# Optimization experiments

Measured on AMD Instinct MI355X. Metric: run time of the kernel, lower is better.

## Reference

```python
import jax, jax.numpy as jnp
import numpy as np

FEAT = 128
N_RBF = 20
CUTOFF = 5.0
NUM_CONV = 3
N_ATOMS = 8000
N_EDGES = 160000
N_MOLS = 100
EPS = 1e-15


def silu(x):
    return x * jax.nn.sigmoid(x)


def setup_inputs() -> dict:
    key = jax.random.key(0)
    ks = jax.random.split(key, 16)
    F = FEAT

    def w(k, shape, fan_in):
        return jax.random.normal(k, shape, dtype=jnp.float32) / np.sqrt(fan_in).astype(np.float32)

    nbr0 = jax.random.randint(ks[12], (N_EDGES,), 0, N_ATOMS)
    # avoid self-edges (would give zero distance)
    nbr1 = (nbr0 + 1 + jax.random.randint(ks[13], (N_EDGES,), 0, N_ATOMS - 1)) % N_ATOMS
    return {
        "xyz": jax.random.uniform(ks[0], (N_ATOMS, 3), dtype=jnp.float32) * 10.0,
        "emb_table": jax.random.normal(ks[1], (100, F), dtype=jnp.float32),
        "msg_w1": w(ks[2], (NUM_CONV, F, F), F),
        "msg_b1": jnp.zeros((NUM_CONV, F), jnp.float32),
        "msg_w2": w(ks[3], (NUM_CONV, F, 3 * F), F),
        "msg_b2": jnp.zeros((NUM_CONV, 3 * F), jnp.float32),
        "rbf_w": w(ks[4], (NUM_CONV, N_RBF, 3 * F), N_RBF),
        "rbf_b": jnp.zeros((NUM_CONV, 3 * F), jnp.float32),
        "upd_u": w(ks[5], (NUM_CONV, F, F), F),
        "upd_v": w(ks[6], (NUM_CONV, F, F), F),
        "upd_w1": w(ks[7], (NUM_CONV, 2 * F, F), 2 * F),
        "upd_b1": jnp.zeros((NUM_CONV, F), jnp.float32),
        "upd_w2": w(ks[8], (NUM_CONV, F, 3 * F), F),
        "upd_b2": jnp.zeros((NUM_CONV, 3 * F), jnp.float32),
        "ro_w1": w(ks[9], (F, F // 2), F),
        "ro_b1": jnp.zeros((F // 2,), jnp.float32),
        "ro_w2": w(ks[10], (F // 2, 1), F // 2),
        "ro_b2": jnp.zeros((1,), jnp.float32),
        "z": jax.random.randint(ks[11], (N_ATOMS,), 0, 100),
        "nbrs": jnp.stack([nbr0, nbr1], axis=1),
        "mol_idx": jnp.sort(jax.random.randint(ks[14], (N_ATOMS,), 0, N_MOLS)),
    }


def painn_forward(xyz, emb_table, msg_w1, msg_b1, msg_w2, msg_b2, rbf_w, rbf_b,
                  upd_u, upd_v, upd_w1, upd_b1, upd_w2, upd_b2,
                  ro_w1, ro_b1, ro_w2, ro_b2, z, nbrs, mol_idx):
    F = FEAT
    N = xyz.shape[0]
    # r_ij points from nbrs[:,0] (center i) to nbrs[:,1] (neighbor j)
    r_ij = xyz[nbrs[:, 1]] - xyz[nbrs[:, 0]]            # (E, 3)
    d = jnp.sqrt(jnp.sum(r_ij * r_ij, axis=-1))         # (E,)
    unit = r_ij / d[:, None]                            # (E, 3)
    # PaiNN sinc radial basis: sin(n*pi*d/cutoff)/d, n = 1..n_rbf
    n = jnp.arange(1, N_RBF + 1, dtype=jnp.float32)
    rbf = jnp.sin(n[None, :] * jnp.pi * d[:, None] / CUTOFF) / d[:, None]  # (E, n_rbf)
    # cosine cutoff envelope
    env = jnp.where(d <= CUTOFF, 0.5 * (jnp.cos(jnp.pi * d / CUTOFF) + 1.0), 0.0)

    s = emb_table[z]                                    # (N, F)
    v = jnp.zeros((N, F, 3), dtype=s.dtype)             # (N, F, 3)

    for i in range(NUM_CONV):
        # ---- message block ----
        phi = silu(s @ msg_w1[i] + msg_b1[i]) @ msg_w2[i] + msg_b2[i]   # (N, 3F)
        w_s = (rbf @ rbf_w[i] + rbf_b[i]) * env[:, None]                # (E, 3F)
        inv = (phi[nbrs[:, 1]] * w_s).reshape(-1, 3, F)                 # (E, 3, F)
        split0 = inv[:, 0, :][..., None]                                # (E, F, 1)
        split1 = inv[:, 1, :]                                           # (E, F)
        split2 = inv[:, 2, :][..., None]                                # (E, F, 1)
        dv_ij = split2 * unit[:, None, :] + split0 * v[nbrs[:, 1]]      # (E, F, 3)
        ds = jax.ops.segment_sum(split1, nbrs[:, 0], num_segments=N)
        dv = jax.ops.segment_sum(dv_ij, nbrs[:, 0], num_segments=N)
        s = s + ds
        v = v + dv
        # ---- update block ----
        u_v = jnp.einsum('nfd,fg->ngd', v, upd_u[i])                    # (N, F, 3)
        v_v = jnp.einsum('nfd,fg->ngd', v, upd_v[i])                    # (N, F, 3)
        v_v_norm = jnp.sqrt(jnp.sum(v_v * v_v, axis=-1) + EPS)          # (N, F)
        stack = jnp.concatenate([s, v_v_norm], axis=-1)                 # (N, 2F)
        a = (silu(stack @ upd_w1[i] + upd_b1[i]) @ upd_w2[i] + upd_b2[i]).reshape(-1, 3, F)
        a_vv = a[:, 0, :][..., None]
        a_sv = a[:, 1, :]
        a_ss = a[:, 2, :]
        dv_u = u_v * a_vv
        ds_u = jnp.sum(u_v * v_v, axis=-1) * a_sv + a_ss
        s = s + ds_u
        v = v + dv_u

    # readout MLP + per-molecule sum pool (SumPool)
    atom_e = silu(s @ ro_w1 + ro_b1) @ ro_w2 + ro_b2                    # (N, 1)
    energy = jax.ops.segment_sum(atom_e, mol_idx, num_segments=N_MOLS)  # (N_MOLS, 1)
    return energy


def reference(xyz, emb_table, msg_w1, msg_b1, msg_w2, msg_b2, rbf_w, rbf_b,
              upd_u, upd_v, upd_w1, upd_b1, upd_w2, upd_b2,
              ro_w1, ro_b1, ro_w2, ro_b2, z, nbrs, mol_idx):
    return painn_forward(xyz, emb_table, msg_w1, msg_b1, msg_w2, msg_b2, rbf_w, rbf_b,
                         upd_u, upd_v, upd_w1, upd_b1, upd_w2, upd_b2,
                         ro_w1, ro_b1, ro_w2, ro_b2, z, nbrs, mol_idx)
```

## Files before the change

kernel.cpp:

```cpp
#include <hip/hip_runtime.h>

static constexpr int F = 128;
static constexpr int N_RBF = 20;
static constexpr int N_ATOMS = 8000;
static constexpr int NP = 8064;
static constexpr int N_EDGES = 160000;
static constexpr int N_MOLS = 100;
static constexpr float CUTOFF = 5.0f;
static constexpr size_t NFC = (size_t)NP * F;
static constexpr int REC = 28;
#define PIF 3.14159265358979323846f

typedef __attribute__((ext_vector_type(8))) short bf16x8;
typedef __attribute__((ext_vector_type(4))) float f32x4;
typedef unsigned short ushort_t;
typedef unsigned int uint_t;

__device__ __forceinline__ float silu_f(float x) { return x / (1.f + __expf(-x)); }

__device__ __forceinline__ ushort_t f2bf(float x) {
    union { float f; uint_t u; } v; v.f = x;
    uint_t r = v.u + 0x7fffu + ((v.u >> 16) & 1u);
    return (ushort_t)(r >> 16);
}
__device__ __forceinline__ float bf2f(ushort_t h) {
    union { uint_t u; float f; } v; v.u = ((uint_t)h) << 16; return v.f;
}

__global__ __launch_bounds__(256) void count_kernel(
    const float* __restrict__ xyz, const int* __restrict__ nbrs,
    float* __restrict__ envb, int* __restrict__ cnt)
{
    int e = blockIdx.x * 256 + threadIdx.x;
    if (e >= N_EDGES) return;
    int i0 = nbrs[2*e+0], i1 = nbrs[2*e+1];
    float dx = xyz[3*i1+0] - xyz[3*i0+0];
    float dy = xyz[3*i1+1] - xyz[3*i0+1];
    float dz = xyz[3*i1+2] - xyz[3*i0+2];
    float d  = sqrtf(dx*dx + dy*dy + dz*dz);
    float ev = (d <= CUTOFF) ? 0.5f*(cosf(PIF*d/CUTOFF) + 1.f) : 0.f;
    envb[e] = ev;
    if (ev > 0.f) atomicAdd(&cnt[i0], 1);
}

__global__ __launch_bounds__(1024) void scan_kernel(
    const int* __restrict__ cnt, int* __restrict__ offsets, float* __restrict__ out)
{
    __shared__ int sums[1024];
    int tid = threadIdx.x;
    if (tid < N_MOLS) out[tid] = 0.f;
    int base = tid * 8;
    int local[8]; int s = 0;
    #pragma unroll
    for (int i = 0; i < 8; ++i) {
        int idx = base + i;
        local[i] = (idx < N_ATOMS) ? cnt[idx] : 0;
        s += local[i];
    }
    sums[tid] = s;
    __syncthreads();
    for (int d = 1; d < 1024; d <<= 1) {
        int v = (tid >= d) ? sums[tid - d] : 0;
        __syncthreads();
        sums[tid] += v;
        __syncthreads();
    }
    int ex = (tid == 0) ? 0 : sums[tid - 1];
    #pragma unroll
    for (int i = 0; i < 8; ++i) {
        int idx = base + i;
        if (idx < N_ATOMS) { offsets[idx] = ex; ex += local[i]; }
    }
}

__global__ __launch_bounds__(256) void build_kernel(
    const float* __restrict__ xyz, const int* __restrict__ nbrs,
    const float* __restrict__ envb, const int* __restrict__ offsets,
    int* __restrict__ cursor, float* __restrict__ rec)
{
    int e = blockIdx.x * 256 + threadIdx.x;
    if (e >= N_EDGES) return;
    float ev = envb[e];
    if (ev <= 0.f) return;
    int i0 = nbrs[2*e+0], i1 = nbrs[2*e+1];
    float dx = xyz[3*i1+0] - xyz[3*i0+0];
    float dy = xyz[3*i1+1] - xyz[3*i0+1];
    float dz = xyz[3*i1+2] - xyz[3*i0+2];
    float d  = sqrtf(dx*dx + dy*dy + dz*dz);
    float inv = 1.f / d;
    int pos = offsets[i0] + atomicAdd(&cursor[i0], 1);
    float* r = rec + (size_t)pos * REC;
    r[0] = __int_as_float(i1);
    r[1] = ev;
    r[2] = dx*inv; r[3] = dy*inv; r[4] = dz*inv;
    float base = PIF*d/CUTOFF;
    float sc = inv * ev;
    #pragma unroll
    for (int k = 0; k < N_RBF; ++k)
        r[5 + k] = sinf((float)(k+1)*base) * sc;
}

static constexpr int WPREP_W = 557056;
static constexpr int WPREP_TOTAL = 557184;
static constexpr int NATF = N_ATOMS * F;
static constexpr int PREP_TOTAL = NATF + WPREP_TOTAL + 2 * N_ATOMS;
__global__ __launch_bounds__(256) void prep_kernel(
    const float* __restrict__ emb, const int* __restrict__ z, float* __restrict__ s,
    const float* __restrict__ msg_w1, const float* __restrict__ msg_w2,
    const float* __restrict__ upd_u,  const float* __restrict__ upd_v,
    const float* __restrict__ upd_w1, const float* __restrict__ upd_w2,
    const float* __restrict__ ro_w1,  const float* __restrict__ ro_b1,
    ushort_t* __restrict__ dhi, ushort_t* __restrict__ dlo,
    float* __restrict__ robias, int* __restrict__ cntz)
{
    int gidx = blockIdx.x * 256 + threadIdx.x;
    if (gidx < NATF) {
        int n = gidx >> 7, f = gidx & 127;
        s[gidx] = emb[z[n]*F + f];
        return;
    }
    int idx = gidx - NATF;
    if (idx >= WPREP_TOTAL) {
        cntz[idx - WPREP_TOTAL] = 0;
        return;
    }
    if (idx >= WPREP_W) {
        int l = idx - WPREP_W;
        robias[l] = (l < 64) ? ro_b1[l] : 0.f;
        return;
    }
    float val;
    if (idx < 540672) {
        const float* src; int K, N, rem;
        if (idx < 49152)       { int l = idx;          int c = l / 16384; rem = l % 16384; K = 128; N = 128; src = msg_w1 + c * 16384; }
        else if (idx < 196608) { int l = idx - 49152;  int c = l / 49152; rem = l % 49152; K = 128; N = 384; src = msg_w2 + c * 49152; }
        else if (idx < 294912) { int l = idx - 196608; int c = l / 32768; rem = l % 32768; K = 128; N = 128;
                                 if (rem < 16384) src = upd_u + c * 16384;
                                 else { src = upd_v + c * 16384; rem -= 16384; } }
        else if (idx < 393216) { int l = idx - 294912; int c = l / 32768; rem = l % 32768; K = 256; N = 128; src = upd_w1 + c * 32768; }
        else                   { int l = idx - 393216; int c = l / 49152; rem = l % 49152; K = 128; N = 384; src = upd_w2 + c * 49152; }
        int n = rem / K, k = rem % K;
        val = src[k * N + n];
    } else {
        int l = idx - 540672;
        int n = l >> 7, k = l & 127;
        val = (n < 64) ? ro_w1[k * 64 + n] : 0.f;
    }
    ushort_t h = f2bf(val);
    dhi[idx] = h;
    dlo[idx] = f2bf(val - bf2f(h));
}

__global__ __launch_bounds__(256) void phi0_kernel(
    const float* __restrict__ sbuf,
    const ushort_t* __restrict__ W1h, const ushort_t* __restrict__ W1l,
    const float* __restrict__ b1,
    const ushort_t* __restrict__ W2h, const ushort_t* __restrict__ W2l,
    const float* __restrict__ b2,
    float* __restrict__ C)
{
    __shared__ __align__(16) ushort_t Ah[2][32 * 40], Al[2][32 * 40];
    __shared__ __align__(16) ushort_t Bh[2][128 * 40], Bl[2][128 * 40];
    __shared__ __align__(16) ushort_t Hh[32 * 136], Hl[32 * 136];
    const int tid = threadIdx.x;
    const int wave = tid >> 6, lane = tid & 63;
    const int row_l = lane & 15, quad = lane >> 4;
    const int wn = wave * 32;
    const int m0 = blockIdx.x * 32;
    const int lrA = tid >> 3, ksA = (tid & 7) * 4;
    const int lrB = tid >> 1, ksB = (tid & 1) * 16;

    float4 rx;
    uint4 b_h0, b_h1, b_l0, b_l1;

    auto loadB1 = [&](int k0) {
        const ushort_t* bh = &W1h[(size_t)lrB * 128 + k0 + ksB];
        const ushort_t* bl = &W1l[(size_t)lrB * 128 + k0 + ksB];
        b_h0 = *(const uint4*)bh; b_h1 = *(const uint4*)(bh + 8);
        b_l0 = *(const uint4*)bl; b_l1 = *(const uint4*)(bl + 8);
    };
    auto loadB2 = [&](int it2) {
        int ct = it2 >> 2, k0 = (it2 & 3) * 32;
        const ushort_t* bh = &W2h[(size_t)(ct * 128 + lrB) * 128 + k0 + ksB];
        const ushort_t* bl = &W2l[(size_t)(ct * 128 + lrB) * 128 + k0 + ksB];
        b_h0 = *(const uint4*)bh; b_h1 = *(const uint4*)(bh + 8);
        b_l0 = *(const uint4*)bl; b_l1 = *(const uint4*)(bl + 8);
    };
    auto writeA = [&](int buf) {
        float e[4] = {rx.x, rx.y, rx.z, rx.w};
        ushort_t ph[4], pl[4];
        #pragma unroll
        for (int t = 0; t < 4; ++t) {
            ushort_t h = f2bf(e[t]);
            ph[t] = h; pl[t] = f2bf(e[t] - bf2f(h));
        }
        *(uint2*)&Ah[buf][lrA * 40 + ksA] = *(uint2*)ph;
        *(uint2*)&Al[buf][lrA * 40 + ksA] = *(uint2*)pl;
    };
    auto writeB = [&](int buf) {
        *(uint4*)&Bh[buf][lrB * 40 + ksB]     = b_h0;
        *(uint4*)&Bh[buf][lrB * 40 + ksB + 8] = b_h1;
        *(uint4*)&Bl[buf][lrB * 40 + ksB]     = b_l0;
        *(uint4*)&Bl[buf][lrB * 40 + ksB + 8] = b_l1;
    };

    f32x4 acc[2][2];
    #pragma unroll
    for (int i = 0; i < 2; ++i)
        #pragma unroll
        for (int j = 0; j < 2; ++j)
            #pragma unroll
            for (int r = 0; r < 4; ++r) acc[i][j][r] = 0.f;

    rx = *(const float4*)&sbuf[(size_t)(m0 + lrA) * 128 + ksA];
    loadB1(0);
    writeA(0); writeB(0);
    __syncthreads();
    #pragma unroll
    for (int it = 0; it < 4; ++it) {
        const int k0n = (it + 1) * 32;
        if (it + 1 < 4) {
            rx = *(const float4*)&sbuf[(size_t)(m0 + lrA) * 128 + k0n + ksA];
            loadB1(k0n);
        }
        bf16x8 ahf[2], alf[2], bhf[2], blf[2];
        #pragma unroll
        for (int i = 0; i < 2; ++i) {
            int ar = (i * 16 + row_l) * 40 + quad * 8;
            ahf[i] = *(const bf16x8*)&Ah[it & 1][ar];
            alf[i] = *(const bf16x8*)&Al[it & 1][ar];
        }
        #pragma unroll
        for (int j = 0; j < 2; ++j) {
            int br = (wn + j * 16 + row_l) * 40 + quad * 8;
            bhf[j] = *(const bf16x8*)&Bh[it & 1][br];
            blf[j] = *(const bf16x8*)&Bl[it & 1][br];
        }
        #pragma unroll
        for (int i = 0; i < 2; ++i)
            #pragma unroll
            for (int j = 0; j < 2; ++j) {
                acc[i][j] = __builtin_amdgcn_mfma_f32_16x16x32_bf16(ahf[i], bhf[j], acc[i][j], 0, 0, 0);
                acc[i][j] = __builtin_amdgcn_mfma_f32_16x16x32_bf16(ahf[i], blf[j], acc[i][j], 0, 0, 0);
                acc[i][j] = __builtin_amdgcn_mfma_f32_16x16x32_bf16(alf[i], bhf[j], acc[i][j], 0, 0, 0);
            }
        if (it + 1 < 4) { writeA((it + 1) & 1); writeB((it + 1) & 1); }
        __syncthreads();
    }
    #pragma unroll
    for (int j = 0; j < 2; ++j) {
        int col = wn + j * 16 + row_l;
        float bval = b1[col];
        #pragma unroll
        for (int i = 0; i < 2; ++i)
            #pragma unroll
            for (int r = 0; r < 4; ++r) {
                int row = i * 16 + quad * 4 + r;
                float v = silu_f(acc[i][j][r] + bval);
                ushort_t h = f2bf(v);
                Hh[row * 136 + col] = h;
                Hl[row * 136 + col] = f2bf(v - bf2f(h));
            }
    }

    #pragma unroll
    for (int i = 0; i < 2; ++i)
        #pragma unroll
        for (int j = 0; j < 2; ++j)
            #pragma unroll
            for (int r = 0; r < 4; ++r) acc[i][j][r] = 0.f;
    loadB2(0); writeB(0);
    __syncthreads();
    #pragma unroll
    for (int it = 0; it < 12; ++it) {
        const int k0 = (it & 3) * 32;
        if (it + 1 < 12) loadB2(it + 1);
        bf16x8 ahf[2], alf[2], bhf[2], blf[2];
        #pragma unroll
        for (int i = 0; i < 2; ++i) {
            int ar = (i * 16 + row_l) * 136 + k0 + quad * 8;
            ahf[i] = *(const bf16x8*)&Hh[ar];
            alf[i] = *(const bf16x8*)&Hl[ar];
        }
        #pragma unroll
        for (int j = 0; j < 2; ++j) {
            int br = (wn + j * 16 + row_l) * 40 + quad * 8;
            bhf[j] = *(const bf16x8*)&Bh[it & 1][br];
            blf[j] = *(const bf16x8*)&Bl[it & 1][br];
        }
        #pragma unroll
        for (int i = 0; i < 2; ++i)
            #pragma unroll
            for (int j = 0; j < 2; ++j) {
                acc[i][j] = __builtin_amdgcn_mfma_f32_16x16x32_bf16(ahf[i], bhf[j], acc[i][j], 0, 0, 0);
                acc[i][j] = __builtin_amdgcn_mfma_f32_16x16x32_bf16(ahf[i], blf[j], acc[i][j], 0, 0, 0);
                acc[i][j] = __builtin_amdgcn_mfma_f32_16x16x32_bf16(alf[i], bhf[j], acc[i][j], 0, 0, 0);
            }
        if ((it & 3) == 3) {
            const int ct = it >> 2;
            #pragma unroll
            for (int j = 0; j < 2; ++j) {
                int col = ct * 128 + wn + j * 16 + row_l;
                float bval = b2[col];
                #pragma unroll
                for (int i = 0; i < 2; ++i)
                    #pragma unroll
                    for (int r = 0; r < 4; ++r) {
                        int row = i * 16 + quad * 4 + r;
                        C[(size_t)(m0 + row) * 384 + col] = acc[i][j][r] + bval;
                    }
            }
            #pragma unroll
            for (int i = 0; i < 2; ++i)
                #pragma unroll
                for (int j = 0; j < 2; ++j)
                    #pragma unroll
                    for (int r = 0; r < 4; ++r) acc[i][j][r] = 0.f;
        }
        if (it + 1 < 12) writeB((it + 1) & 1);
        __syncthreads();
    }
}

template<int TAIL>
__global__ __launch_bounds__(256) void updphi_kernel(
    float* __restrict__ s_io, float* __restrict__ v_io,
    const ushort_t* __restrict__ UVh, const ushort_t* __restrict__ UVl,
    const ushort_t* __restrict__ W1h, const ushort_t* __restrict__ W1l,
    const float* __restrict__ b1,
    const ushort_t* __restrict__ W2h, const ushort_t* __restrict__ W2l,
    const float* __restrict__ b2,
    const ushort_t* __restrict__ XW1h, const ushort_t* __restrict__ XW1l,
    const float* __restrict__ xb1,
    const ushort_t* __restrict__ XW2h, const ushort_t* __restrict__ XW2l,
    const float* __restrict__ xb2,
    float* __restrict__ phi_out,
    const float* __restrict__ w2ro, const float* __restrict__ b2ro,
    const int* __restrict__ mol, float* __restrict__ outp)
{
    __shared__ float uvv[96][260];
    __shared__ __align__(16) ushort_t Bh[2][128 * 40];
    __shared__ __align__(16) ushort_t Bl[2][128 * 40];
    __shared__ __align__(16) unsigned char AH[17408];
    __shared__ float molacc[128];
    __shared__ float redl[32][4];
    const int tid = threadIdx.x;
    const int wave = tid >> 6, lane = tid & 63;
    const int row_l = lane & 15, quad = lane >> 4;
    const int wn = wave * 32;
    const int m0 = blockIdx.x * 32;
    const int lrA = tid >> 3;
    const int ksA = (tid & 7) * 4;
    const int lrB = tid >> 1, ksB = (tid & 1) * 16;

    float* sS = &uvv[0][0];
    constexpr int SSTR = 132;

    {
        ushort_t* A0h = (ushort_t*)AH;
        ushort_t* A0l = A0h + 96 * 40;
        ushort_t* B0h = &Bh[0][0];
        ushort_t* B0l = &Bl[0][0];
        f32x4 acc0[6][4];
        #pragma unroll
        for (int i = 0; i < 6; ++i)
            #pragma unroll
            for (int j = 0; j < 4; ++j)
                #pragma unroll
                for (int r = 0; r < 4; ++r) acc0[i][j][r] = 0.f;
        for (int k0 = 0; k0 < 128; k0 += 32) {
            #pragma unroll
            for (int g = 0; g < 3; ++g) {
                int row = g * 32 + lrA;
                float4 v = *(const float4*)&v_io[(size_t)(m0 * 3 + row) * 128 + k0 + ksA];
                float e[4] = {v.x, v.y, v.z, v.w};
                ushort_t ph[4], pl[4];
                #pragma unroll
                for (int t = 0; t < 4; ++t) {
                    ushort_t h = f2bf(e[t]);
                    ph[t] = h; pl[t] = f2bf(e[t] - bf2f(h));
                }
                *(uint2*)&A0h[row * 40 + ksA] = *(uint2*)ph;
                *(uint2*)&A0l[row * 40 + ksA] = *(uint2*)pl;
            }
            {
                const ushort_t* bh = &UVh[(size_t)tid * 128 + k0];
                const ushort_t* bl = &UVl[(size_t)tid * 128 + k0];
                *(uint4*)&B0h[tid * 40 + 0]  = *(const uint4*)(bh + 0);
                *(uint4*)&B0h[tid * 40 + 8]  = *(const uint4*)(bh + 8);
                *(uint4*)&B0h[tid * 40 + 16] = *(const uint4*)(bh + 16);
                *(uint4*)&B0h[tid * 40 + 24] = *(const uint4*)(bh + 24);
                *(uint4*)&B0l[tid * 40 + 0]  = *(const uint4*)(bl + 0);
                *(uint4*)&B0l[tid * 40 + 8]  = *(const uint4*)(bl + 8);
                *(uint4*)&B0l[tid * 40 + 16] = *(const uint4*)(bl + 16);
                *(uint4*)&B0l[tid * 40 + 24] = *(const uint4*)(bl + 24);
            }
            __syncthreads();
            bf16x8 a0h[6], a0l[6], b0h[4], b0l[4];
            #pragma unroll
            for (int i = 0; i < 6; ++i) {
                int ar = (i * 16 + row_l) * 40 + quad * 8;
                a0h[i] = *(const bf16x8*)&A0h[ar];
                a0l[i] = *(const bf16x8*)&A0l[ar];
            }
            #pragma unroll
            for (int j = 0; j < 4; ++j) {
                int br = (wave * 64 + j * 16 + row_l) * 40 + quad * 8;
                b0h[j] = *(const bf16x8*)&B0h[br];
                b0l[j] = *(const bf16x8*)&B0l[br];
            }
            #pragma unroll
            for (int i = 0; i < 6; ++i)
                #pragma unroll
                for (int j = 0; j < 4; ++j) {
                    acc0[i][j] = __builtin_amdgcn_mfma_f32_16x16x32_bf16(a0h[i], b0h[j], acc0[i][j], 0, 0, 0);
                    acc0[i][j] = __builtin_amdgcn_mfma_f32_16x16x32_bf16(a0h[i], b0l[j], acc0[i][j], 0, 0, 0);
                    acc0[i][j] = __builtin_amdgcn_mfma_f32_16x16x32_bf16(a0l[i], b0h[j], acc0[i][j], 0, 0, 0);
                }
            __syncthreads();
        }
        #pragma unroll
        for (int i = 0; i < 6; ++i)
            #pragma unroll
            for (int j = 0; j < 4; ++j)
                #pragma unroll
                for (int r = 0; r < 4; ++r)
                    uvv[i * 16 + quad * 4 + r][wave * 64 + j * 16 + row_l] = acc0[i][j][r];
        __syncthreads();
    }

    ushort_t* Ah1 = (ushort_t*)AH;
    ushort_t* Al1 = Ah1 + 2 * 32 * 40;
    ushort_t* Hh  = (ushort_t*)AH;
    ushort_t* Hl  = Hh + 32 * 136;

    float4 rx;
    uint4 b_h0, b_h1, b_l0, b_l1;

    auto loadB1 = [&](int k0) {
        const ushort_t* bh = &W1h[(size_t)lrB * 256 + k0 + ksB];
        const ushort_t* bl = &W1l[(size_t)lrB * 256 + k0 + ksB];
        b_h0 = *(const uint4*)bh; b_h1 = *(const uint4*)(bh + 8);
        b_l0 = *(const uint4*)bl; b_l1 = *(const uint4*)(bl + 8);
    };
    auto writeB = [&](int buf) {
        *(uint4*)&Bh[buf][lrB * 40 + ksB]     = b_h0;
        *(uint4*)&Bh[buf][lrB * 40 + ksB + 8] = b_h1;
        *(uint4*)&Bl[buf][lrB * 40 + ksB]     = b_l0;
        *(uint4*)&Bl[buf][lrB * 40 + ksB + 8] = b_l1;
    };
    auto writeA1 = [&](int buf, int k0) {
        float e[4];
        if (k0 < 128) {
            e[0] = rx.x; e[1] = rx.y; e[2] = rx.z; e[3] = rx.w;
        } else {
            int f = k0 + ksA;
            #pragma unroll
            for (int t = 0; t < 4; ++t) {
                float x = uvv[lrA * 3 + 0][f + t];
                float y = uvv[lrA * 3 + 1][f + t];
                float z = uvv[lrA * 3 + 2][f + t];
                e[t] = sqrtf(x * x + y * y + z * z + 1e-15f);
            }
        }
        ushort_t ph[4], pl[4];
        #pragma unroll
        for (int t = 0; t < 4; ++t) {
            ushort_t h = f2bf(e[t]);
            ph[t] = h; pl[t] = f2bf(e[t] - bf2f(h));
        }
        *(uint2*)&Ah1[buf * 1280 + lrA * 40 + ksA] = *(uint2*)ph;
        *(uint2*)&Al1[buf * 1280 + lrA * 40 + ksA] = *(uint2*)pl;
    };

    f32x4 acc[2][2];
    #pragma unroll
    for (int i = 0; i < 2; ++i)
        #pragma unroll
        for (int j = 0; j < 2; ++j)
            #pragma unroll
            for (int r = 0; r < 4; ++r) acc[i][j][r] = 0.f;

    rx = *(const float4*)&s_io[(size_t)(m0 + lrA) * 128 + ksA];
    loadB1(0);
    writeA1(0, 0); writeB(0);
    __syncthreads();
    #pragma unroll
    for (int it = 0; it < 8; ++it) {
        const int k0n = (it + 1) * 32;
        if (it + 1 < 8) {
            if (k0n < 128) rx = *(const float4*)&s_io[(size_t)(m0 + lrA) * 128 + k0n + ksA];
            loadB1(k0n);
        }
        bf16x8 ahf[2], alf[2], bhf[2], blf[2];
        #pragma unroll
        for (int i = 0; i < 2; ++i) {
            int ar = (i * 16 + row_l) * 40 + quad * 8;
            ahf[i] = *(const bf16x8*)&Ah1[(it & 1) * 1280 + ar];
            alf[i] = *(const bf16x8*)&Al1[(it & 1) * 1280 + ar];
        }
        #pragma unroll
        for (int j = 0; j < 2; ++j) {
            int br = (wn + j * 16 + row_l) * 40 + quad * 8;
            bhf[j] = *(const bf16x8*)&Bh[it & 1][br];
            blf[j] = *(const bf16x8*)&Bl[it & 1][br];
        }
        #pragma unroll
        for (int i = 0; i < 2; ++i)
            #pragma unroll
            for (int j = 0; j < 2; ++j) {
                acc[i][j] = __builtin_amdgcn_mfma_f32_16x16x32_bf16(ahf[i], bhf[j], acc[i][j], 0, 0, 0);
                acc[i][j] = __builtin_amdgcn_mfma_f32_16x16x32_bf16(ahf[i], blf[j], acc[i][j], 0, 0, 0);
                acc[i][j] = __builtin_amdgcn_mfma_f32_16x16x32_bf16(alf[i], bhf[j], acc[i][j], 0, 0, 0);
            }
        if (it + 1 < 8) { writeA1((it + 1) & 1, k0n); writeB((it + 1) & 1); }
        __syncthreads();
    }
    #pragma unroll
    for (int j = 0; j < 2; ++j) {
        int col = wn + j * 16 + row_l;
        float bval = b1[col];
        #pragma unroll
        for (int i = 0; i < 2; ++i)
            #pragma unroll
            for (int r = 0; r < 4; ++r) {
                int row = i * 16 + quad * 4 + r;
                float v = silu_f(acc[i][j][r] + bval);
                ushort_t h = f2bf(v);
                Hh[row * 136 + col] = h;
                Hl[row * 136 + col] = f2bf(v - bf2f(h));
            }
    }

    constexpr int CT0 = TAIL ? 1 : 0;
    constexpr int NIT2 = (3 - CT0) * 4;
    auto loadB2 = [&](int it2) {
        int ct = CT0 + (it2 >> 2), k0 = (it2 & 3) * 32;
        const ushort_t* bh = &W2h[(size_t)(ct * 128 + lrB) * 128 + k0 + ksB];
        const ushort_t* bl = &W2l[(size_t)(ct * 128 + lrB) * 128 + k0 + ksB];
        b_h0 = *(const uint4*)bh; b_h1 = *(const uint4*)(bh + 8);
        b_l0 = *(const uint4*)bl; b_l1 = *(const uint4*)(bl + 8);
    };

    #pragma unroll
    for (int i = 0; i < 2; ++i)
        #pragma unroll
        for (int j = 0; j < 2; ++j)
            #pragma unroll
            for (int r = 0; r < 4; ++r) acc[i][j][r] = 0.f;
    f32x4 ssum[2][2];

    loadB2(0); writeB(0);
    __syncthreads();
    #pragma unroll
    for (int it = 0; it < NIT2; ++it) {
        const int k0 = (it & 3) * 32;
        if (it + 1 < NIT2) loadB2(it + 1);
        bf16x8 ahf[2], alf[2], bhf[2], blf[2];
        #pragma unroll
        for (int i = 0; i < 2; ++i) {
            int ar = (i * 16 + row_l) * 136 + k0 + quad * 8;
            ahf[i] = *(const bf16x8*)&Hh[ar];
            alf[i] = *(const bf16x8*)&Hl[ar];
        }
        #pragma unroll
        for (int j = 0; j < 2; ++j) {
            int br = (wn + j * 16 + row_l) * 40 + quad * 8;
            bhf[j] = *(const bf16x8*)&Bh[it & 1][br];
            blf[j] = *(const bf16x8*)&Bl[it & 1][br];
        }
        #pragma unroll
        for (int i = 0; i < 2; ++i)
            #pragma unroll
            for (int j = 0; j < 2; ++j) {
                acc[i][j] = __builtin_amdgcn_mfma_f32_16x16x32_bf16(ahf[i], bhf[j], acc[i][j], 0, 0, 0);
                acc[i][j] = __builtin_amdgcn_mfma_f32_16x16x32_bf16(ahf[i], blf[j], acc[i][j], 0, 0, 0);
                acc[i][j] = __builtin_amdgcn_mfma_f32_16x16x32_bf16(alf[i], bhf[j], acc[i][j], 0, 0, 0);
            }
        if ((it & 3) == 3) {
            const int ct = CT0 + (it >> 2);
            #pragma unroll
            for (int j = 0; j < 2; ++j) {
                int f = wn + j * 16 + row_l;
                float bval = b2[ct * 128 + f];
                #pragma unroll
                for (int i = 0; i < 2; ++i)
                    #pragma unroll
                    for (int r = 0; r < 4; ++r) {
                        int ln = i * 16 + quad * 4 + r;
                        float a = acc[i][j][r] + bval;
                        if (ct == 0) {
                            size_t vb = (size_t)(m0 + ln) * 3 * F + f;
                            v_io[vb]         += uvv[ln * 3 + 0][f] * a;
                            v_io[vb + F]     += uvv[ln * 3 + 1][f] * a;
                            v_io[vb + 2 * F] += uvv[ln * 3 + 2][f] * a;
                        } else if (ct == 1) {
                            float dot = uvv[ln * 3 + 0][f] * uvv[ln * 3 + 0][128 + f]
                                      + uvv[ln * 3 + 1][f] * uvv[ln * 3 + 1][128 + f]
                                      + uvv[ln * 3 + 2][f] * uvv[ln * 3 + 2][128 + f];
                            ssum[i][j][r] = dot * a;
                        } else {
                            float sv = s_io[(size_t)(m0 + ln) * F + f] + ssum[i][j][r] + a;
                            if constexpr (TAIL == 0) s_io[(size_t)(m0 + ln) * F + f] = sv;
                            sS[ln * SSTR + f] = sv;
                        }
                    }
            }
            #pragma unroll
            for (int i = 0; i < 2; ++i)
                #pragma unroll
                for (int j = 0; j < 2; ++j)
                    #pragma unroll
                    for (int r = 0; r < 4; ++r) acc[i][j][r] = 0.f;
        }
        if (it + 1 < NIT2) writeB((it + 1) & 1);
        __syncthreads();
    }

    if constexpr (TAIL == 1) { if (tid < 128) molacc[tid] = 0.f; }
    ushort_t* Ah3 = (ushort_t*)AH;
    ushort_t* Al3 = Ah3 + 2 * 1280;

    auto loadB31 = [&](int k0) {
        const ushort_t* bh = &XW1h[(size_t)lrB * 128 + k0 + ksB];
        const ushort_t* bl = &XW1l[(size_t)lrB * 128 + k0 + ksB];
        b_h0 = *(const uint4*)bh; b_h1 = *(const uint4*)(bh + 8);
        b_l0 = *(const uint4*)bl; b_l1 = *(const uint4*)(bl + 8);
    };
    auto writeA3 = [&](int buf, int k0) {
        float e[4];
        #pragma unroll
        for (int t = 0; t < 4; ++t) e[t] = sS[lrA * SSTR + k0 + ksA + t];
        ushort_t ph[4], pl[4];
        #pragma unroll
        for (int t = 0; t < 4; ++t) {
            ushort_t h = f2bf(e[t]);
            ph[t] = h; pl[t] = f2bf(e[t] - bf2f(h));
        }
        *(uint2*)&Ah3[buf * 1280 + lrA * 40 + ksA] = *(uint2*)ph;
        *(uint2*)&Al3[buf * 1280 + lrA * 40 + ksA] = *(uint2*)pl;
    };

    #pragma unroll
    for (int i = 0; i < 2; ++i)
        #pragma unroll
        for (int j = 0; j < 2; ++j)
            #pragma unroll
            for (int r = 0; r < 4; ++r) acc[i][j][r] = 0.f;

    loadB31(0);
    writeA3(0, 0); writeB(0);
    __syncthreads();
    #pragma unroll
    for (int it = 0; it < 4; ++it) {
        const int k0n = (it + 1) * 32;
        if (it + 1 < 4) loadB31(k0n);
        bf16x8 ahf[2], alf[2], bhf[2], blf[2];
        #pragma unroll
        for (int i = 0; i < 2; ++i) {
            int ar = (i * 16 + row_l) * 40 + quad * 8;
            ahf[i] = *(const bf16x8*)&Ah3[(it & 1) * 1280 + ar];
            alf[i] = *(const bf16x8*)&Al3[(it & 1) * 1280 + ar];
        }
        #pragma unroll
        for (int j = 0; j < 2; ++j) {
            int br = (wn + j * 16 + row_l) * 40 + quad * 8;
            bhf[j] = *(const bf16x8*)&Bh[it & 1][br];
            blf[j] = *(const bf16x8*)&Bl[it & 1][br];
        }
        #pragma unroll
        for (int i = 0; i < 2; ++i)
            #pragma unroll
            for (int j = 0; j < 2; ++j) {
                acc[i][j] = __builtin_amdgcn_mfma_f32_16x16x32_bf16(ahf[i], bhf[j], acc[i][j], 0, 0, 0);
                acc[i][j] = __builtin_amdgcn_mfma_f32_16x16x32_bf16(ahf[i], blf[j], acc[i][j], 0, 0, 0);
                acc[i][j] = __builtin_amdgcn_mfma_f32_16x16x32_bf16(alf[i], bhf[j], acc[i][j], 0, 0, 0);
            }
        if (it + 1 < 4) { writeA3((it + 1) & 1, k0n); writeB((it + 1) & 1); }
        __syncthreads();
    }

    if constexpr (TAIL == 0) {
        #pragma unroll
        for (int j = 0; j < 2; ++j) {
            int col = wn + j * 16 + row_l;
            float bval = xb1[col];
            #pragma unroll
            for (int i = 0; i < 2; ++i)
                #pragma unroll
                for (int r = 0; r < 4; ++r) {
                    int row = i * 16 + quad * 4 + r;
                    float v = silu_f(acc[i][j][r] + bval);
                    ushort_t h = f2bf(v);
                    Hh[row * 136 + col] = h;
                    Hl[row * 136 + col] = f2bf(v - bf2f(h));
                }
        }
        auto loadB32 = [&](int it2) {
            int ct = it2 >> 2, k0 = (it2 & 3) * 32;
            const ushort_t* bh = &XW2h[(size_t)(ct * 128 + lrB) * 128 + k0 + ksB];
            const ushort_t* bl = &XW2l[(size_t)(ct * 128 + lrB) * 128 + k0 + ksB];
            b_h0 = *(const uint4*)bh; b_h1 = *(const uint4*)(bh + 8);
            b_l0 = *(const uint4*)bl; b_l1 = *(const uint4*)(bl + 8);
        };
        #pragma unroll
        for (int i = 0; i < 2; ++i)
            #pragma unroll
            for (int j = 0; j < 2; ++j)
                #pragma unroll
                for (int r = 0; r < 4; ++r) acc[i][j][r] = 0.f;
        loadB32(0); writeB(0);
        __syncthreads();
        #pragma unroll
        for (int it = 0; it < 12; ++it) {
            const int k0 = (it & 3) * 32;
            if (it + 1 < 12) loadB32(it + 1);
            bf16x8 ahf[2], alf[2], bhf[2], blf[2];
            #pragma unroll
            for (int i = 0; i < 2; ++i) {
                int ar = (i * 16 + row_l) * 136 + k0 + quad * 8;
                ahf[i] = *(const bf16x8*)&Hh[ar];
                alf[i] = *(const bf16x8*)&Hl[ar];
            }
            #pragma unroll
            for (int j = 0; j < 2; ++j) {
                int br = (wn + j * 16 + row_l) * 40 + quad * 8;
                bhf[j] = *(const bf16x8*)&Bh[it & 1][br];
                blf[j] = *(const bf16x8*)&Bl[it & 1][br];
            }
            #pragma unroll
            for (int i = 0; i < 2; ++i)
                #pragma unroll
                for (int j = 0; j < 2; ++j) {
                    acc[i][j] = __builtin_amdgcn_mfma_f32_16x16x32_bf16(ahf[i], bhf[j], acc[i][j], 0, 0, 0);
                    acc[i][j] = __builtin_amdgcn_mfma_f32_16x16x32_bf16(ahf[i], blf[j], acc[i][j], 0, 0, 0);
                    acc[i][j] = __builtin_amdgcn_mfma_f32_16x16x32_bf16(alf[i], bhf[j], acc[i][j], 0, 0, 0);
                }
            if ((it & 3) == 3) {
                const int ct = it >> 2;
                #pragma unroll
                for (int j = 0; j < 2; ++j) {
                    int col = ct * 128 + wn + j * 16 + row_l;
                    float bval = xb2[col];
                    #pragma unroll
                    for (int i = 0; i < 2; ++i)
                        #pragma unroll
                        for (int r = 0; r < 4; ++r) {
                            int row = i * 16 + quad * 4 + r;
                            phi_out[(size_t)(m0 + row) * 384 + col] = acc[i][j][r] + bval;
                        }
                }
                #pragma unroll
                for (int i = 0; i < 2; ++i)
                    #pragma unroll
                    for (int j = 0; j < 2; ++j)
                        #pragma unroll
                        for (int r = 0; r < 4; ++r) acc[i][j][r] = 0.f;
            }
            if (it + 1 < 12) writeB((it + 1) & 1);
            __syncthreads();
        }
    } else {
        float part[2][4];
        #pragma unroll
        for (int i = 0; i < 2; ++i)
            #pragma unroll
            for (int r = 0; r < 4; ++r) part[i][r] = 0.f;
        #pragma unroll
        for (int j = 0; j < 2; ++j) {
            int col = wn + j * 16 + row_l;
            float bv = xb1[col];
            float wv = (col < 64) ? w2ro[col] : 0.f;
            #pragma unroll
            for (int i = 0; i < 2; ++i)
                #pragma unroll
                for (int r = 0; r < 4; ++r)
                    part[i][r] += silu_f(acc[i][j][r] + bv) * wv;
        }
        #pragma unroll
        for (int o = 1; o < 16; o <<= 1)
            #pragma unroll
            for (int i = 0; i < 2; ++i)
                #pragma unroll
                for (int r = 0; r < 4; ++r)
                    part[i][r] += __shfl_xor(part[i][r], o);
        if (row_l == 0)
            #pragma unroll
            for (int i = 0; i < 2; ++i)
                #pragma unroll
                for (int r = 0; r < 4; ++r)
                    redl[i * 16 + quad * 4 + r][wave] = part[i][r];
        __syncthreads();
        if (tid < 32) {
            int n = m0 + tid;
            if (n < N_ATOMS) {
                float e = redl[tid][0] + redl[tid][1] + redl[tid][2] + redl[tid][3] + b2ro[0];
                atomicAdd(&molacc[mol[n]], e);
            }
        }
        __syncthreads();
        if (tid < 100 && molacc[tid] != 0.f) atomicAdd(&outp[tid], molacc[tid]);
    }
}

template<int ZVIN>
__global__ __launch_bounds__(128) void msg_gather(
    const float* __restrict__ phi, const float* __restrict__ rec,
    const float* __restrict__ rbf_w, const float* __restrict__ rbf_b,
    const float* __restrict__ v_in, float* __restrict__ s,
    float* __restrict__ v_out, const int* __restrict__ offsets,
    const int* __restrict__ cnt)
{
    const int n = blockIdx.x, tid = threadIdx.x;
    float W0[N_RBF], W1[N_RBF], W2[N_RBF];
    #pragma unroll
    for (int k = 0; k < N_RBF; ++k) {
        W0[k] = rbf_w[k*3*F + tid];
        W1[k] = rbf_w[k*3*F + F + tid];
        W2[k] = rbf_w[k*3*F + 2*F + tid];
    }
    const float b0 = rbf_b[tid], b1 = rbf_b[F + tid], b2 = rbf_b[2*F + tid];
    float ds = 0.f, dvx = 0.f, dvy = 0.f, dvz = 0.f;
    const int off = offsets[n], c = cnt[n];
    const float* r = rec + (size_t)off * REC;
    #pragma unroll 2
    for (int t = 0; t < c; ++t, r += REC) {
        int j = __float_as_int(r[0]);
        float ev = r[1];
        float ux = r[2], uy = r[3], uz = r[4];
        float w0 = b0 * ev, w1 = b1 * ev, w2 = b2 * ev;
        #pragma unroll
        for (int k = 0; k < N_RBF; ++k) {
            float rk = r[5 + k];
            w0 += rk * W0[k]; w1 += rk * W1[k]; w2 += rk * W2[k];
        }
        const float* prow = phi + (size_t)j * 3 * F;
        float s0 = prow[tid] * w0;
        float s1 = prow[F + tid] * w1;
        float s2 = prow[2*F + tid] * w2;
        ds  += s1;
        if constexpr (ZVIN) {
            dvx += s2*ux; dvy += s2*uy; dvz += s2*uz;
        } else {
            const float* vrow = v_in + (size_t)j * 3 * F;
            dvx += s2*ux + s0 * vrow[tid];
            dvy += s2*uy + s0 * vrow[F + tid];
            dvz += s2*uz + s0 * vrow[2*F + tid];
        }
    }
    s[(size_t)n * F + tid] += ds;
    size_t vb = (size_t)n * 3 * F + tid;
    if constexpr (ZVIN) {
        v_out[vb]       = dvx;
        v_out[vb + F]   = dvy;
        v_out[vb + 2*F] = dvz;
    } else {
        v_out[vb]       = v_in[vb]       + dvx;
        v_out[vb + F]   = v_in[vb + F]   + dvy;
        v_out[vb + 2*F] = v_in[vb + 2*F] + dvz;
    }
}

extern "C" void kernel_launch(void* const* d_in, const int* in_sizes, int n_in,
                              void* d_out, int out_size, void* d_ws, size_t ws_size,
                              hipStream_t stream)
{
    const float* xyz    = (const float*)d_in[0];
    const float* emb    = (const float*)d_in[1];
    const float* msg_w1 = (const float*)d_in[2];
    const float* msg_b1 = (const float*)d_in[3];
    const float* msg_w2 = (const float*)d_in[4];
    const float* msg_b2 = (const float*)d_in[5];
    const float* rbf_w  = (const float*)d_in[6];
    const float* rbf_b  = (const float*)d_in[7];
    const float* upd_u  = (const float*)d_in[8];
    const float* upd_v  = (const float*)d_in[9];
    const float* upd_w1 = (const float*)d_in[10];
    const float* upd_b1 = (const float*)d_in[11];
    const float* upd_w2 = (const float*)d_in[12];
    const float* upd_b2 = (const float*)d_in[13];
    const float* ro_w1  = (const float*)d_in[14];
    const float* ro_b1  = (const float*)d_in[15];
    const float* ro_w2  = (const float*)d_in[16];
    const float* ro_b2  = (const float*)d_in[17];
    const int*   z      = (const int*)d_in[18];
    const int*   nbrs   = (const int*)d_in[19];
    const int*   molidx = (const int*)d_in[20];
    float* out = (float*)d_out;

    float* ws = (float*)d_ws;
    size_t off = 0;
    auto alloc = [&](size_t n) { float* p = ws + off; off += n; return p; };
    float* s_buf   = alloc(NFC);
    float* v1_buf  = alloc(3 * NFC);
    float* v2_buf  = alloc(3 * NFC);
    float* phi_buf = alloc(3 * NFC);
    float* envb    = alloc(N_EDGES);
    float* edgerec = alloc((size_t)N_EDGES * REC);
    ushort_t* wbf_hi = (ushort_t*)alloc(WPREP_W / 2 + 64);
    ushort_t* wbf_lo = (ushort_t*)alloc(WPREP_W / 2 + 64);
    float* robias   = alloc(128);
    int* cnt        = (int*)alloc(N_ATOMS);
    int* cursor     = (int*)alloc(N_ATOMS);
    int* offsets    = (int*)alloc(N_ATOMS);

    const size_t oW1 = 0, oW2 = 49152, oUV = 196608, oU1 = 294912, oU2 = 393216, oRO = 540672;

    prep_kernel<<<dim3(PREP_TOTAL / 256), dim3(256), 0, stream>>>(
        emb, z, s_buf,
        msg_w1, msg_w2, upd_u, upd_v, upd_w1, upd_w2, ro_w1, ro_b1,
        wbf_hi, wbf_lo, robias, cnt);
    count_kernel<<<dim3((N_EDGES + 255) / 256), dim3(256), 0, stream>>>(
        xyz, nbrs, envb, cnt);
    scan_kernel<<<dim3(1), dim3(1024), 0, stream>>>(cnt, offsets, out);
    build_kernel<<<dim3((N_EDGES + 255) / 256), dim3(256), 0, stream>>>(
        xyz, nbrs, envb, offsets, cursor, edgerec);

    phi0_kernel<<<dim3(NP/32), dim3(256), 0, stream>>>(
        s_buf,
        wbf_hi + oW1, wbf_lo + oW1, msg_b1,
        wbf_hi + oW2, wbf_lo + oW2, msg_b2,
        phi_buf);

    float* vin = v1_buf;
    float* vout = v2_buf;
    for (int i = 0; i < 3; ++i) {
        if (i == 0)
            msg_gather<1><<<dim3(N_ATOMS), dim3(128), 0, stream>>>(
                phi_buf, edgerec, rbf_w + (size_t)i*N_RBF*3*F, rbf_b + (size_t)i*3*F,
                vin, s_buf, vout, offsets, cnt);
        else
            msg_gather<0><<<dim3(N_ATOMS), dim3(128), 0, stream>>>(
                phi_buf, edgerec, rbf_w + (size_t)i*N_RBF*3*F, rbf_b + (size_t)i*3*F,
                vin, s_buf, vout, offsets, cnt);
        if (i < 2) {
            updphi_kernel<0><<<dim3(NP/32), dim3(256), 0, stream>>>(
                s_buf, vout,
                wbf_hi + oUV + (size_t)i*32768, wbf_lo + oUV + (size_t)i*32768,
                wbf_hi + oU1 + (size_t)i*32768, wbf_lo + oU1 + (size_t)i*32768,
                upd_b1 + (size_t)i*F,
                wbf_hi + oU2 + (size_t)i*49152, wbf_lo + oU2 + (size_t)i*49152,
                upd_b2 + (size_t)i*3*F,
                wbf_hi + oW1 + (size_t)(i+1)*16384, wbf_lo + oW1 + (size_t)(i+1)*16384,
                msg_b1 + (size_t)(i+1)*F,
                wbf_hi + oW2 + (size_t)(i+1)*49152, wbf_lo + oW2 + (size_t)(i+1)*49152,
                msg_b2 + (size_t)(i+1)*3*F,
                phi_buf,
                nullptr, nullptr, nullptr, nullptr);
        } else {
            updphi_kernel<1><<<dim3(NP/32), dim3(256), 0, stream>>>(
                s_buf, vout,
                wbf_hi + oUV + (size_t)i*32768, wbf_lo + oUV + (size_t)i*32768,
                wbf_hi + oU1 + (size_t)i*32768, wbf_lo + oU1 + (size_t)i*32768,
                upd_b1 + (size_t)i*F,
                wbf_hi + oU2 + (size_t)i*49152, wbf_lo + oU2 + (size_t)i*49152,
                upd_b2 + (size_t)i*3*F,
                wbf_hi + oRO, wbf_lo + oRO, robias,
                nullptr, nullptr, nullptr,
                nullptr,
                ro_w2, ro_b2, molidx, out);
        }
        float* tmp = vin; vin = vout; vout = tmp;
    }
}
```

Baseline: 327.8 us.

## Merge edge build into phi0 launch and deepen weight prefetch to two stages

Merges the edge-record build kernel into the phi0 GEMM kernel as extra blocks, so the two independent workloads share one launch and run concurrently. The update kernel's B-weight global loads now prefetch two iterations ahead through double register buffers, and the message-gather edge loop is unrolled four times instead of two. This aims to hide global load latency and cut launch gaps, at the cost of more registers per thread, which may reduce occupancy. The build blocks also carry the GEMM kernel's shared memory allocation.

```diff
diff --git a/kernel.cpp b/kernel.cpp
--- a/kernel.cpp
+++ b/kernel.cpp
@@ -9,6 +9,8 @@
 static constexpr float CUTOFF = 5.0f;
 static constexpr size_t NFC = (size_t)NP * F;
 static constexpr int REC = 28;
+static constexpr int NPHI_BLK = NP / 32;
+static constexpr int NBUILD_BLK = (N_EDGES + 255) / 256;
 #define PIF 3.14159265358979323846f
 
 typedef __attribute__((ext_vector_type(8))) short bf16x8;
@@ -26,6 +28,7 @@
 __device__ __forceinline__ float bf2f(ushort_t h) {
     union { uint_t u; float f; } v; v.u = ((uint_t)h) << 16; return v.f;
 }
+
 
 __global__ __launch_bounds__(256) void count_kernel(
     const float* __restrict__ xyz, const int* __restrict__ nbrs,
@@ -71,33 +74,6 @@
         int idx = base + i;
         if (idx < N_ATOMS) { offsets[idx] = ex; ex += local[i]; }
     }
-}
-
-__global__ __launch_bounds__(256) void build_kernel(
-    const float* __restrict__ xyz, const int* __restrict__ nbrs,
-    const float* __restrict__ envb, const int* __restrict__ offsets,
-    int* __restrict__ cursor, float* __restrict__ rec)
-{
-    int e = blockIdx.x * 256 + threadIdx.x;
-    if (e >= N_EDGES) return;
-    float ev = envb[e];
-    if (ev <= 0.f) return;
-    int i0 = nbrs[2*e+0], i1 = nbrs[2*e+1];
-    float dx = xyz[3*i1+0] - xyz[3*i0+0];
-    float dy = xyz[3*i1+1] - xyz[3*i0+1];
-    float dz = xyz[3*i1+2] - xyz[3*i0+2];
-    float d  = sqrtf(dx*dx + dy*dy + dz*dz);
-    float inv = 1.f / d;
-    int pos = offsets[i0] + atomicAdd(&cursor[i0], 1);
-    float* r = rec + (size_t)pos * REC;
-    r[0] = __int_as_float(i1);
-    r[1] = ev;
-    r[2] = dx*inv; r[3] = dy*inv; r[4] = dz*inv;
-    float base = PIF*d/CUTOFF;
-    float sc = inv * ev;
-    #pragma unroll
-    for (int k = 0; k < N_RBF; ++k)
-        r[5 + k] = sinf((float)(k+1)*base) * sc;
 }
 
 static constexpr int WPREP_W = 557056;
@@ -151,7 +127,10 @@
     dlo[idx] = f2bf(val - bf2f(h));
 }
 
-__global__ __launch_bounds__(256) void phi0_kernel(
+__global__ __launch_bounds__(256) void build_phi0_kernel(
+    const float* __restrict__ xyz, const int* __restrict__ nbrs,
+    const float* __restrict__ envb, const int* __restrict__ offsets,
+    int* __restrict__ cursor, float* __restrict__ rec,
     const float* __restrict__ sbuf,
     const ushort_t* __restrict__ W1h, const ushort_t* __restrict__ W1l,
     const float* __restrict__ b1,
@@ -159,6 +138,30 @@
     const float* __restrict__ b2,
     float* __restrict__ C)
 {
+    if (blockIdx.x >= NPHI_BLK) {
+        int e = (blockIdx.x - NPHI_BLK) * 256 + threadIdx.x;
+        if (e >= N_EDGES) return;
+        float ev = envb[e];
+        if (ev <= 0.f) return;
+        int i0 = nbrs[2*e+0], i1 = nbrs[2*e+1];
+        float dx = xyz[3*i1+0] - xyz[3*i0+0];
+        float dy = xyz[3*i1+1] - xyz[3*i0+1];
+        float dz = xyz[3*i1+2] - xyz[3*i0+2];
+        float d  = sqrtf(dx*dx + dy*dy + dz*dz);
+        float inv = 1.f / d;
+        int pos = offsets[i0] + atomicAdd(&cursor[i0], 1);
+        float* r = rec + (size_t)pos * REC;
+        r[0] = __int_as_float(i1);
+        r[1] = ev;
+        r[2] = dx*inv; r[3] = dy*inv; r[4] = dz*inv;
+        float base = PIF*d/CUTOFF;
+        float sc = inv * ev;
+        #pragma unroll
+        for (int k = 0; k < N_RBF; ++k)
+            r[5 + k] = sinf((float)(k+1)*base) * sc;
+        return;
+    }
+
     __shared__ __align__(16) ushort_t Ah[2][32 * 40], Al[2][32 * 40];
     __shared__ __align__(16) ushort_t Bh[2][128 * 40], Bl[2][128 * 40];
     __shared__ __align__(16) ushort_t Hh[32 * 136], Hl[32 * 136];
@@ -436,18 +439,25 @@
 
     float4 rx;
     uint4 b_h0, b_h1, b_l0, b_l1;
-
-    auto loadB1 = [&](int k0) {
-        const ushort_t* bh = &W1h[(size_t)lrB * 256 + k0 + ksB];
-        const ushort_t* bl = &W1l[(size_t)lrB * 256 + k0 + ksB];
-        b_h0 = *(const uint4*)bh; b_h1 = *(const uint4*)(bh + 8);
-        b_l0 = *(const uint4*)bl; b_l1 = *(const uint4*)(bl + 8);
-    };
+    uint4 bqh0[2], bqh1[2], bql0[2], bql1[2];
+
     auto writeB = [&](int buf) {
         *(uint4*)&Bh[buf][lrB * 40 + ksB]     = b_h0;
         *(uint4*)&Bh[buf][lrB * 40 + ksB + 8] = b_h1;
         *(uint4*)&Bl[buf][lrB * 40 + ksB]     = b_l0;
         *(uint4*)&Bl[buf][lrB * 40 + ksB + 8] = b_l1;
+    };
+    auto writeBq = [&](int p) {
+        *(uint4*)&Bh[p][lrB * 40 + ksB]     = bqh0[p];
+        *(uint4*)&Bh[p][lrB * 40 + ksB + 8] = bqh1[p];
+        *(uint4*)&Bl[p][lrB * 40 + ksB]     = bql0[p];
+        *(uint4*)&Bl[p][lrB * 40 + ksB + 8] = bql1[p];
+    };
+    auto loadB1q = [&](int k0, int p) {
+        const ushort_t* bh = &W1h[(size_t)lrB * 256 + k0 + ksB];
+        const ushort_t* bl = &W1l[(size_t)lrB * 256 + k0 + ksB];
+        bqh0[p] = *(const uint4*)bh; bqh1[p] = *(const uint4*)(bh + 8);
+        bql0[p] = *(const uint4*)bl; bql1[p] = *(const uint4*)(bl + 8);
     };
     auto writeA1 = [&](int buf, int k0) {
         float e[4];
@@ -482,22 +492,22 @@
             for (int r = 0; r < 4; ++r) acc[i][j][r] = 0.f;
 
     rx = *(const float4*)&s_io[(size_t)(m0 + lrA) * 128 + ksA];
-    loadB1(0);
-    writeA1(0, 0); writeB(0);
+    loadB1q(0, 0);
+    writeA1(0, 0); writeBq(0);
+    loadB1q(32, 1);
     __syncthreads();
     #pragma unroll
     for (int it = 0; it < 8; ++it) {
         const int k0n = (it + 1) * 32;
-        if (it + 1 < 8) {
-            if (k0n < 128) rx = *(const float4*)&s_io[(size_t)(m0 + lrA) * 128 + k0n + ksA];
-            loadB1(k0n);
-        }
+        if (it + 2 < 8) loadB1q((it + 2) * 32, it & 1);
+        if (it + 1 < 8 && k0n < 128)
+            rx = *(const float4*)&s_io[(size_t)(m0 + lrA) * 128 + k0n + ksA];
         bf16x8 ahf[2], alf[2], bhf[2], blf[2];
         #pragma unroll
         for (int i = 0; i < 2; ++i) {
-            int ar = (i * 16 + row_l) * 40 + quad * 8;
-            ahf[i] = *(const bf16x8*)&Ah1[(it & 1) * 1280 + ar];
-            alf[i] = *(const bf16x8*)&Al1[(it & 1) * 1280 + ar];
+            int ar = (it & 1) * 1280 + (i * 16 + row_l) * 40 + quad * 8;
+            ahf[i] = *(const bf16x8*)&Ah1[ar];
+            alf[i] = *(const bf16x8*)&Al1[ar];
         }
         #pragma unroll
         for (int j = 0; j < 2; ++j) {
@@ -513,7 +523,7 @@
                 acc[i][j] = __builtin_amdgcn_mfma_f32_16x16x32_bf16(ahf[i], blf[j], acc[i][j], 0, 0, 0);
                 acc[i][j] = __builtin_amdgcn_mfma_f32_16x16x32_bf16(alf[i], bhf[j], acc[i][j], 0, 0, 0);
             }
-        if (it + 1 < 8) { writeA1((it + 1) & 1, k0n); writeB((it + 1) & 1); }
+        if (it + 1 < 8) { writeA1((it + 1) & 1, k0n); writeBq((it + 1) & 1); }
         __syncthreads();
     }
     #pragma unroll
@@ -534,12 +544,12 @@
 
     constexpr int CT0 = TAIL ? 1 : 0;
     constexpr int NIT2 = (3 - CT0) * 4;
-    auto loadB2 = [&](int it2) {
+    auto loadB2q = [&](int it2, int p) {
         int ct = CT0 + (it2 >> 2), k0 = (it2 & 3) * 32;
         const ushort_t* bh = &W2h[(size_t)(ct * 128 + lrB) * 128 + k0 + ksB];
         const ushort_t* bl = &W2l[(size_t)(ct * 128 + lrB) * 128 + k0 + ksB];
-        b_h0 = *(const uint4*)bh; b_h1 = *(const uint4*)(bh + 8);
-        b_l0 = *(const uint4*)bl; b_l1 = *(const uint4*)(bl + 8);
+        bqh0[p] = *(const uint4*)bh; bqh1[p] = *(const uint4*)(bh + 8);
+        bql0[p] = *(const uint4*)bl; bql1[p] = *(const uint4*)(bl + 8);
     };
 
     #pragma unroll
@@ -550,12 +560,13 @@
             for (int r = 0; r < 4; ++r) acc[i][j][r] = 0.f;
     f32x4 ssum[2][2];
 
-    loadB2(0); writeB(0);
+    loadB2q(0, 0); writeBq(0);
+    loadB2q(1, 1);
     __syncthreads();
     #pragma unroll
     for (int it = 0; it < NIT2; ++it) {
         const int k0 = (it & 3) * 32;
-        if (it + 1 < NIT2) loadB2(it + 1);
+        if (it + 2 < NIT2) loadB2q(it + 2, it & 1);
         bf16x8 ahf[2], alf[2], bhf[2], blf[2];
         #pragma unroll
         for (int i = 0; i < 2; ++i) {
@@ -613,7 +624,7 @@
                     #pragma unroll
                     for (int r = 0; r < 4; ++r) acc[i][j][r] = 0.f;
         }
-        if (it + 1 < NIT2) writeB((it + 1) & 1);
+        if (it + 1 < NIT2) writeBq((it + 1) & 1);
         __syncthreads();
     }
 
@@ -658,9 +669,9 @@
         bf16x8 ahf[2], alf[2], bhf[2], blf[2];
         #pragma unroll
         for (int i = 0; i < 2; ++i) {
-            int ar = (i * 16 + row_l) * 40 + quad * 8;
-            ahf[i] = *(const bf16x8*)&Ah3[(it & 1) * 1280 + ar];
-            alf[i] = *(const bf16x8*)&Al3[(it & 1) * 1280 + ar];
+            int ar = (it & 1) * 1280 + (i * 16 + row_l) * 40 + quad * 8;
+            ahf[i] = *(const bf16x8*)&Ah3[ar];
+            alf[i] = *(const bf16x8*)&Al3[ar];
         }
         #pragma unroll
         for (int j = 0; j < 2; ++j) {
@@ -696,12 +707,12 @@
                     Hl[row * 136 + col] = f2bf(v - bf2f(h));
                 }
         }
-        auto loadB32 = [&](int it2) {
+        auto loadB32q = [&](int it2, int p) {
             int ct = it2 >> 2, k0 = (it2 & 3) * 32;
             const ushort_t* bh = &XW2h[(size_t)(ct * 128 + lrB) * 128 + k0 + ksB];
             const ushort_t* bl = &XW2l[(size_t)(ct * 128 + lrB) * 128 + k0 + ksB];
-            b_h0 = *(const uint4*)bh; b_h1 = *(const uint4*)(bh + 8);
-            b_l0 = *(const uint4*)bl; b_l1 = *(const uint4*)(bl + 8);
+            bqh0[p] = *(const uint4*)bh; bqh1[p] = *(const uint4*)(bh + 8);
+            bql0[p] = *(const uint4*)bl; bql1[p] = *(const uint4*)(bl + 8);
         };
         #pragma unroll
         for (int i = 0; i < 2; ++i)
@@ -709,12 +720,13 @@
             for (int j = 0; j < 2; ++j)
                 #pragma unroll
                 for (int r = 0; r < 4; ++r) acc[i][j][r] = 0.f;
-        loadB32(0); writeB(0);
+        loadB32q(0, 0); writeBq(0);
+        loadB32q(1, 1);
         __syncthreads();
         #pragma unroll
         for (int it = 0; it < 12; ++it) {
             const int k0 = (it & 3) * 32;
-            if (it + 1 < 12) loadB32(it + 1);
+            if (it + 2 < 12) loadB32q(it + 2, it & 1);
             bf16x8 ahf[2], alf[2], bhf[2], blf[2];
             #pragma unroll
             for (int i = 0; i < 2; ++i) {
@@ -757,7 +769,7 @@
                         #pragma unroll
                         for (int r = 0; r < 4; ++r) acc[i][j][r] = 0.f;
             }
-            if (it + 1 < 12) writeB((it + 1) & 1);
+            if (it + 1 < 12) writeBq((it + 1) & 1);
             __syncthreads();
         }
     } else {
@@ -823,7 +835,7 @@
     float ds = 0.f, dvx = 0.f, dvy = 0.f, dvz = 0.f;
     const int off = offsets[n], c = cnt[n];
     const float* r = rec + (size_t)off * REC;
-    #pragma unroll 2
+    #pragma unroll 4
     for (int t = 0; t < c; ++t, r += REC) {
         int j = __float_as_int(r[0]);
         float ev = r[1];
@@ -906,17 +918,15 @@
 
     const size_t oW1 = 0, oW2 = 49152, oUV = 196608, oU1 = 294912, oU2 = 393216, oRO = 540672;
 
-    prep_kernel<<<dim3(PREP_TOTAL / 256), dim3(256), 0, stream>>>(
+    prep_kernel<<<dim3((PREP_TOTAL + 255) / 256), dim3(256), 0, stream>>>(
         emb, z, s_buf,
         msg_w1, msg_w2, upd_u, upd_v, upd_w1, upd_w2, ro_w1, ro_b1,
         wbf_hi, wbf_lo, robias, cnt);
     count_kernel<<<dim3((N_EDGES + 255) / 256), dim3(256), 0, stream>>>(
         xyz, nbrs, envb, cnt);
     scan_kernel<<<dim3(1), dim3(1024), 0, stream>>>(cnt, offsets, out);
-    build_kernel<<<dim3((N_EDGES + 255) / 256), dim3(256), 0, stream>>>(
-        xyz, nbrs, envb, offsets, cursor, edgerec);
-
-    phi0_kernel<<<dim3(NP/32), dim3(256), 0, stream>>>(
+    build_phi0_kernel<<<dim3(NPHI_BLK + NBUILD_BLK), dim3(256), 0, stream>>>(
+        xyz, nbrs, envb, offsets, cursor, edgerec,
         s_buf,
         wbf_hi + oW1, wbf_lo + oW1, msg_b1,
         wbf_hi + oW2, wbf_lo + oW2, msg_b2,
```

Result: slower. 384.7 us (+17.4%).
